# Optimization experiments

Hardware: AMD Instinct MI355X
Metric: run time of the kernel (lower is better)

Reference implementation:

```python
import jax, jax.numpy as jnp
import numpy as np

B, L, K, T, C_IN, C_OUT, TKS = 32, 1855, 7, 40, 8, 32, 5


def setup_inputs() -> dict:
    key = jax.random.key(0)
    k1, k2, k3, k4 = jax.random.split(key, 4)
    x = jax.random.normal(k1, (B, L, T, C_IN), dtype=jnp.float32)
    idx = jax.random.randint(k2, (L, K), 0, L, dtype=jnp.int32)
    missing = jax.random.uniform(k3, (L, K)) < 0.1
    neighbor_indices = jnp.where(missing, jnp.int32(-1), idx)
    fan_in = K * TKS * C_IN
    fan_out = K * TKS * C_OUT
    limit = np.sqrt(6.0 / (fan_in + fan_out))  # glorot uniform
    kernel = jax.random.uniform(k4, (K, TKS, C_IN, C_OUT), dtype=jnp.float32,
                                minval=-limit, maxval=limit)
    bias = jnp.zeros((C_OUT,), dtype=jnp.float32)
    return {"x": x, "neighbor_indices": neighbor_indices, "kernel": kernel, "bias": bias}


def reference(x, neighbor_indices, kernel, bias):
    # x: (B, L, T, C_in); neighbor_indices: (L, K) with -1 = missing
    mask = (neighbor_indices != -1)
    safe_idx = jnp.where(mask, neighbor_indices, 0)
    # gather neighbor features: (B, L, K, T, C_in)
    nf = x[:, safe_idx]
    nf = nf * mask[None, :, :, None, None].astype(x.dtype)
    tks = kernel.shape[1]
    t_out = x.shape[2] - tks + 1
    # valid temporal conv: sum over small fixed tau instead of materializing
    # the (B, L, K, T_out, tks, C_in) framed tensor
    out = jnp.zeros((x.shape[0], x.shape[1], t_out, kernel.shape[-1]), dtype=x.dtype)
    for tau in range(tks):
        out = out + jnp.einsum('blkti,kio->blto',
                               nf[:, :, :, tau:tau + t_out, :], kernel[:, tau])
    return out + bias
```

## Files before the change

### kernel.cpp

```cpp
#include <hip/hip_runtime.h>

constexpr int Bn = 32, Ln = 1855, Kn = 7, Tn = 40, CIn = 8, COn = 32, TKSn = 5, TOn = 36;
constexpr int BG   = 8;
constexpr int KRED = Kn * TKSn * CIn;
constexpr int KPAD = 288;
constexpr int WROW = 296;
constexpr int XS_ELEMS = BG * Kn * Tn * CIn;
constexpr int XS2 = 4 * Kn * Tn * CIn;
constexpr size_t XN = (size_t)Bn * Ln * Tn * CIn;

constexpr size_t WS_WT   = 0;
constexpr size_t WS_ZPAD = 18432;
constexpr size_t WS_XBF  = 18560;
constexpr size_t WS_NEED = WS_XBF + XN * 2;

typedef __attribute__((ext_vector_type(8))) short bf16x8;
typedef __attribute__((ext_vector_type(8))) unsigned short u16x8;
typedef __attribute__((ext_vector_type(4))) float f32x4;

__device__ inline unsigned short f2bf(float f) {
    unsigned u = __builtin_bit_cast(unsigned, f);
    u += 0x7fffu + ((u >> 16) & 1u);
    return (unsigned short)(u >> 16);
}

__device__ inline void gload_lds16(const void* g, void* lds) {
    __builtin_amdgcn_global_load_lds(
        (const __attribute__((address_space(1))) unsigned int*)g,
        (__attribute__((address_space(3))) unsigned int*)lds,
        16, 0, 0);
}

__global__ __launch_bounds__(256) void prep_all(const float* __restrict__ x,
                                                unsigned short* __restrict__ xbf,
                                                const float* __restrict__ w,
                                                unsigned short* __restrict__ wt,
                                                unsigned short* __restrict__ zpad) {
    const int tid = threadIdx.x;
    if (blockIdx.x == 2048) {
        for (int p = tid; p < KRED * COn; p += 256) {
            int o  = p & 31;
            int kr = p >> 5;
            wt[o * KPAD + kr] = f2bf(w[p]);
        }
        for (int p = tid; p < COn * (KPAD - KRED); p += 256) {
            int o = p >> 3;
            wt[o * KPAD + KRED + (p & 7)] = 0;
        }
        if (tid < 64) zpad[tid] = 0;
        return;
    }
    const size_t n8 = XN / 8;
    for (size_t p = (size_t)blockIdx.x * 256 + tid; p < n8; p += (size_t)2048 * 256) {
        float4 a = ((const float4*)x)[2 * p];
        float4 b = ((const float4*)x)[2 * p + 1];
        u16x8 v;
        v[0] = f2bf(a.x); v[1] = f2bf(a.y); v[2] = f2bf(a.z); v[3] = f2bf(a.w);
        v[4] = f2bf(b.x); v[5] = f2bf(b.y); v[6] = f2bf(b.z); v[7] = f2bf(b.w);
        *(u16x8*)&xbf[p * 8] = v;
    }
}

template<int NT>
__device__ __forceinline__ void do_tiles(
    int rt0, const unsigned short* __restrict__ xs,
    const bf16x8 (&bfrag)[2][9], float bv0, float bv1,
    float* __restrict__ out, int b0, int l, int quad, int lrow)
{
    f32x4 acc[NT][2];
    int base[NT];
    #pragma unroll
    for (int i = 0; i < NT; ++i) {
        acc[i][0] = f32x4{0.f,0.f,0.f,0.f};
        acc[i][1] = f32x4{0.f,0.f,0.f,0.f};
        const int m  = (rt0 + i) * 16 + lrow;
        const int bl = m / 36, t = m - bl * 36;
        base[i] = bl * 2240 + t * 8;
    }
    __builtin_amdgcn_s_setprio(1);
    #pragma unroll
    for (int c = 0; c < 9; ++c) {
        const int p = c * 4 + quad;
        const int knbr = p / 5, tau = p - knbr * 5;
        const int koff = knbr * 320 + tau * 8;
        #pragma unroll
        for (int i = 0; i < NT; ++i) {
            int o = base[i] + koff;
            if (c == 8 && quad == 3) o = XS2;
            bf16x8 a = *(const bf16x8*)&xs[o];
            acc[i][0] = __builtin_amdgcn_mfma_f32_16x16x32_bf16(a, bfrag[0][c], acc[i][0], 0, 0, 0);
            acc[i][1] = __builtin_amdgcn_mfma_f32_16x16x32_bf16(a, bfrag[1][c], acc[i][1], 0, 0, 0);
        }
    }
    __builtin_amdgcn_s_setprio(0);
    #pragma unroll
    for (int i = 0; i < NT; ++i) {
        #pragma unroll
        for (int reg = 0; reg < 4; ++reg) {
            const int m  = (rt0 + i) * 16 + quad * 4 + reg;
            const int bl = m / 36, t = m - bl * 36;
            const size_t off =
                (((size_t)(b0 + bl) * Ln + l) * TOn + t) * COn + lrow;
            __builtin_nontemporal_store(acc[i][0][reg] + bv0, &out[off]);
            __builtin_nontemporal_store(acc[i][1][reg] + bv1, &out[off + 16]);
        }
    }
}

__global__ __launch_bounds__(128, 4) void conv_mfma5(
    const unsigned short* __restrict__ xbf,
    const int*   __restrict__ nbr,
    const unsigned short* __restrict__ wt,
    const unsigned short* __restrict__ zpad,
    const float* __restrict__ bias,
    float*       __restrict__ out)
{
    __shared__ unsigned short xs[XS2 + 8];

    const int tid  = threadIdx.x;
    const int wave = tid >> 6;
    const int lane = tid & 63;
    const int l    = blockIdx.x;
    const int b0   = blockIdx.y * 4;

    if (tid < 8) xs[XS2 + tid] = 0;

    int nv = 0;
    if (lane < Kn) nv = nbr[l * Kn + lane];

    #pragma unroll
    for (int ch = wave; ch < 18; ch += 2) {
        if (ch < 17 || lane < 32) {
            const int u   = ch * 64 + lane;
            const int row = u / 40;
            const int q   = u - row * 40;
            const int bl  = row / 7;
            const int k   = row - bl * 7;
            const int l2  = __shfl(nv, k);
            const unsigned short* src = zpad;
            if (l2 >= 0)
                src = xbf + ((size_t)(b0 + bl) * Ln + l2) * 320 + q * 8;
            gload_lds16(src, &xs[ch * 512]);
        }
    }

    const int quad = lane >> 4;
    const int lrow = lane & 15;

    bf16x8 bfrag[2][9];
    #pragma unroll
    for (int oh = 0; oh < 2; ++oh)
        #pragma unroll
        for (int c = 0; c < 9; ++c)
            bfrag[oh][c] = *(const bf16x8*)(wt + (oh * 16 + lrow) * KPAD + c * 32 + quad * 8);
    const float bv0 = bias[lrow];
    const float bv1 = bias[16 + lrow];

    __syncthreads();

    if (wave == 0) {
        do_tiles<3>(0, xs, bfrag, bv0, bv1, out, b0, l, quad, lrow);
        do_tiles<2>(3, xs, bfrag, bv0, bv1, out, b0, l, quad, lrow);
    } else {
        do_tiles<3>(5, xs, bfrag, bv0, bv1, out, b0, l, quad, lrow);
        do_tiles<1>(8, xs, bfrag, bv0, bv1, out, b0, l, quad, lrow);
    }
}

__global__ __launch_bounds__(256) void conv_mfma(
    const float* __restrict__ x, const int* __restrict__ nbr,
    const float* __restrict__ w, const float* __restrict__ bias,
    float* __restrict__ out)
{
    __shared__ unsigned short xs[XS_ELEMS + 8];
    __shared__ unsigned short wt[COn * WROW];

    const int tid = threadIdx.x;
    const int l   = blockIdx.x;
    const int bg  = blockIdx.y;

    for (int p = tid; p < KRED * COn; p += 256) {
        int o  = p & 31;
        int kr = p >> 5;
        wt[o * WROW + kr] = f2bf(w[p]);
    }
    for (int p = tid; p < COn * (WROW - KRED); p += 256) {
        int o = p >> 4;
        wt[o * WROW + KRED + (p & 15)] = 0;
    }
    if (tid < 8) xs[XS_ELEMS + tid] = 0;

    for (int p = tid; p < BG * Kn * 80; p += 256) {
        int b_local = p / 560;
        int r = p - b_local * 560;
        int k = r / 80;
        int q = r - k * 80;
        int l2 = nbr[l * Kn + k];
        float4 v = make_float4(0.f, 0.f, 0.f, 0.f);
        if (l2 >= 0)
            v = ((const float4*)x)[((size_t)(bg * BG + b_local) * Ln + l2) * 80 + q];
        ushort4 pk;
        pk.x = f2bf(v.x); pk.y = f2bf(v.y); pk.z = f2bf(v.z); pk.w = f2bf(v.w);
        *(ushort4*)&xs[p * 4] = pk;
    }
    __syncthreads();

    const int wave = tid >> 6;
    const int lane = tid & 63;
    const int quad = lane >> 4;
    const int lrow = lane & 15;
    const int o_base  = (wave & 1) * 16;
    const int rt_base = (wave >> 1) * 9;

    bf16x8 bfrag[9];
    #pragma unroll
    for (int c = 0; c < 9; ++c)
        bfrag[c] = *(const bf16x8*)&wt[(o_base + lrow) * WROW + c * 32 + quad * 8];

    const float bv = bias[o_base + lrow];

    #pragma unroll
    for (int g = 0; g < 3; ++g) {
        const int rt0 = rt_base + g * 3;
        f32x4 acc0 = {0.f,0.f,0.f,0.f}, acc1 = acc0, acc2 = acc0;
        const int m0 = (rt0 + 0) * 16 + lrow;
        const int m1 = (rt0 + 1) * 16 + lrow;
        const int m2 = (rt0 + 2) * 16 + lrow;
        const int bl0 = m0 / 36, t0 = m0 - bl0 * 36;
        const int bl1 = m1 / 36, t1 = m1 - bl1 * 36;
        const int bl2 = m2 / 36, t2 = m2 - bl2 * 36;
        const int base0 = bl0 * 2240 + t0 * 8;
        const int base1 = bl1 * 2240 + t1 * 8;
        const int base2 = bl2 * 2240 + t2 * 8;
        #pragma unroll
        for (int c = 0; c < 9; ++c) {
            const int p = c * 4 + quad;
            const int knbr = p / 5, tau = p - knbr * 5;
            const int koff = knbr * 320 + tau * 8;
            int o0 = base0 + koff, o1 = base1 + koff, o2 = base2 + koff;
            if (c == 8 && quad == 3) { o0 = XS_ELEMS; o1 = XS_ELEMS; o2 = XS_ELEMS; }
            bf16x8 a0 = *(const bf16x8*)&xs[o0];
            bf16x8 a1 = *(const bf16x8*)&xs[o1];
            bf16x8 a2 = *(const bf16x8*)&xs[o2];
            acc0 = __builtin_amdgcn_mfma_f32_16x16x32_bf16(a0, bfrag[c], acc0, 0, 0, 0);
            acc1 = __builtin_amdgcn_mfma_f32_16x16x32_bf16(a1, bfrag[c], acc1, 0, 0, 0);
            acc2 = __builtin_amdgcn_mfma_f32_16x16x32_bf16(a2, bfrag[c], acc2, 0, 0, 0);
        }
        #pragma unroll
        for (int i = 0; i < 3; ++i) {
            const f32x4 acc = (i == 0) ? acc0 : ((i == 1) ? acc1 : acc2);
            const int rt = rt0 + i;
            #pragma unroll
            for (int reg = 0; reg < 4; ++reg) {
                const int m  = rt * 16 + quad * 4 + reg;
                const int bl = m / 36, t = m - bl * 36;
                const size_t off =
                    (((size_t)(bg * BG + bl) * Ln + l) * TOn + t) * COn + o_base + lrow;
                out[off] = acc[reg] + bv;
            }
        }
    }
}

extern "C" void kernel_launch(void* const* d_in, const int* in_sizes, int n_in,
                              void* d_out, int out_size, void* d_ws, size_t ws_size,
                              hipStream_t stream) {
    const float* x    = (const float*)d_in[0];
    const int*   nbr  = (const int*)d_in[1];
    const float* w    = (const float*)d_in[2];
    const float* bias = (const float*)d_in[3];
    float*       out  = (float*)d_out;

    if (ws_size >= WS_NEED && d_ws != nullptr) {
        unsigned short* wt   = (unsigned short*)((char*)d_ws + WS_WT);
        unsigned short* zpad = (unsigned short*)((char*)d_ws + WS_ZPAD);
        unsigned short* xbf  = (unsigned short*)((char*)d_ws + WS_XBF);
        prep_all<<<2049, 256, 0, stream>>>(x, xbf, w, wt, zpad);
        conv_mfma5<<<dim3(Ln, 8), dim3(128), 0, stream>>>(xbf, nbr, wt, zpad, bias, out);
    } else {
        conv_mfma<<<dim3(Ln, Bn / BG), dim3(256), 0, stream>>>(x, nbr, w, bias, out);
    }
}
```

Baseline: 419.0 us.

## Use single-wave blocks over two batches, replacing barrier with vmcnt wait

Each block is now one 64-lane wave handling 2 batch items instead of two waves handling 4. The 72 output rows are covered by 5 MFMA row tiles, with a half-used tail tile that skips stores for the unused lanes. Because the block is a single wave, __syncthreads is replaced by an s_waitcnt vmcnt(0) after the direct global-to-LDS loads. This doubles the grid size and shrinks LDS per block, aiming for more resident blocks and less barrier cost. In exchange, each block reloads the weight fragments and neighbor indices for half as much work, and the tail tile wastes some MFMA throughput.

```diff
diff --git a/kernel.cpp b/kernel.cpp
--- a/kernel.cpp
+++ b/kernel.cpp
@@ -6,7 +6,8 @@
 constexpr int KPAD = 288;
 constexpr int WROW = 296;
 constexpr int XS_ELEMS = BG * Kn * Tn * CIn;
-constexpr int XS2 = 4 * Kn * Tn * CIn;
+constexpr int XB  = 2;
+constexpr int XS3 = XB * Kn * Tn * CIn;
 constexpr size_t XN = (size_t)Bn * Ln * Tn * CIn;
 
 constexpr size_t WS_WT   = 0;
@@ -61,9 +62,9 @@
     }
 }
 
-template<int NT>
-__device__ __forceinline__ void do_tiles(
-    int rt0, const unsigned short* __restrict__ xs,
+template<int RT0, int NT, bool TAIL>
+__device__ __forceinline__ void do_tiles6(
+    const unsigned short* __restrict__ xs,
     const bf16x8 (&bfrag)[2][9], float bv0, float bv1,
     float* __restrict__ out, int b0, int l, int quad, int lrow)
 {
@@ -73,7 +74,9 @@
     for (int i = 0; i < NT; ++i) {
         acc[i][0] = f32x4{0.f,0.f,0.f,0.f};
         acc[i][1] = f32x4{0.f,0.f,0.f,0.f};
-        const int m  = (rt0 + i) * 16 + lrow;
+        int m;
+        if (TAIL && i == NT - 1) m = 64 + (lrow & 7);
+        else                     m = (RT0 + i) * 16 + lrow;
         const int bl = m / 36, t = m - bl * 36;
         base[i] = bl * 2240 + t * 8;
     }
@@ -86,7 +89,7 @@
         #pragma unroll
         for (int i = 0; i < NT; ++i) {
             int o = base[i] + koff;
-            if (c == 8 && quad == 3) o = XS2;
+            if (c == 8 && quad == 3) o = XS3;
             bf16x8 a = *(const bf16x8*)&xs[o];
             acc[i][0] = __builtin_amdgcn_mfma_f32_16x16x32_bf16(a, bfrag[0][c], acc[i][0], 0, 0, 0);
             acc[i][1] = __builtin_amdgcn_mfma_f32_16x16x32_bf16(a, bfrag[1][c], acc[i][1], 0, 0, 0);
@@ -95,9 +98,11 @@
     __builtin_amdgcn_s_setprio(0);
     #pragma unroll
     for (int i = 0; i < NT; ++i) {
+        const bool tail_tile = TAIL && (i == NT - 1);
+        if (tail_tile && quad >= 2) continue;
         #pragma unroll
         for (int reg = 0; reg < 4; ++reg) {
-            const int m  = (rt0 + i) * 16 + quad * 4 + reg;
+            const int m  = (RT0 + i) * 16 + quad * 4 + reg;
             const int bl = m / 36, t = m - bl * 36;
             const size_t off =
                 (((size_t)(b0 + bl) * Ln + l) * TOn + t) * COn + lrow;
@@ -107,7 +112,7 @@
     }
 }
 
-__global__ __launch_bounds__(128, 4) void conv_mfma5(
+__global__ __launch_bounds__(64, 3) void conv_mfma6(
     const unsigned short* __restrict__ xbf,
     const int*   __restrict__ nbr,
     const unsigned short* __restrict__ wt,
@@ -115,23 +120,21 @@
     const float* __restrict__ bias,
     float*       __restrict__ out)
 {
-    __shared__ unsigned short xs[XS2 + 8];
-
-    const int tid  = threadIdx.x;
-    const int wave = tid >> 6;
-    const int lane = tid & 63;
+    __shared__ unsigned short xs[XS3 + 8];
+
+    const int lane = threadIdx.x;
     const int l    = blockIdx.x;
-    const int b0   = blockIdx.y * 4;
-
-    if (tid < 8) xs[XS2 + tid] = 0;
+    const int b0   = blockIdx.y * XB;
+
+    if (lane < 8) xs[XS3 + lane] = 0;
 
     int nv = 0;
     if (lane < Kn) nv = nbr[l * Kn + lane];
 
     #pragma unroll
-    for (int ch = wave; ch < 18; ch += 2) {
-        if (ch < 17 || lane < 32) {
-            const int u   = ch * 64 + lane;
+    for (int s = 0; s < 9; ++s) {
+        if (s < 8 || lane < 48) {
+            const int u   = s * 64 + lane;
             const int row = u / 40;
             const int q   = u - row * 40;
             const int bl  = row / 7;
@@ -140,7 +143,7 @@
             const unsigned short* src = zpad;
             if (l2 >= 0)
                 src = xbf + ((size_t)(b0 + bl) * Ln + l2) * 320 + q * 8;
-            gload_lds16(src, &xs[ch * 512]);
+            gload_lds16(src, &xs[s * 512]);
         }
     }
 
@@ -156,15 +159,10 @@
     const float bv0 = bias[lrow];
     const float bv1 = bias[16 + lrow];
 
-    __syncthreads();
-
-    if (wave == 0) {
-        do_tiles<3>(0, xs, bfrag, bv0, bv1, out, b0, l, quad, lrow);
-        do_tiles<2>(3, xs, bfrag, bv0, bv1, out, b0, l, quad, lrow);
-    } else {
-        do_tiles<3>(5, xs, bfrag, bv0, bv1, out, b0, l, quad, lrow);
-        do_tiles<1>(8, xs, bfrag, bv0, bv1, out, b0, l, quad, lrow);
-    }
+    asm volatile("s_waitcnt vmcnt(0)" ::: "memory");
+
+    do_tiles6<0, 3, false>(xs, bfrag, bv0, bv1, out, b0, l, quad, lrow);
+    do_tiles6<3, 2, true >(xs, bfrag, bv0, bv1, out, b0, l, quad, lrow);
 }
 
 __global__ __launch_bounds__(256) void conv_mfma(
@@ -276,7 +274,7 @@
         unsigned short* zpad = (unsigned short*)((char*)d_ws + WS_ZPAD);
         unsigned short* xbf  = (unsigned short*)((char*)d_ws + WS_XBF);
         prep_all<<<2049, 256, 0, stream>>>(x, xbf, w, wt, zpad);
-        conv_mfma5<<<dim3(Ln, 8), dim3(128), 0, stream>>>(xbf, nbr, wt, zpad, bias, out);
+        conv_mfma6<<<dim3(Ln, Bn / XB), dim3(64), 0, stream>>>(xbf, nbr, wt, zpad, bias, out);
     } else {
         conv_mfma<<<dim3(Ln, Bn / BG), dim3(256), 0, stream>>>(x, nbr, w, bias, out);
     }
```

After: 363.4 us. 13.3% less time.
